# Performance work log

Hardware: AMD Instinct MI355X
Metric: run time of the kernel (lower is better)

The kernel has to match this reference:

```python
import jax, jax.numpy as jnp
import numpy as np

N_NODES = 50000
N_EDGES = 800000
IN_F = 256
OUT_F = 64


def setup_inputs() -> dict:
    key = jax.random.key(0)
    k1, k2, k3, k4, k5 = jax.random.split(key, 5)
    x = jax.random.normal(k1, (N_NODES, IN_F), dtype=jnp.float32)
    # xavier-uniform-like init for weight
    limit = float(np.sqrt(6.0 / (IN_F + OUT_F)))
    weight = jax.random.uniform(k2, (IN_F, OUT_F), dtype=jnp.float32, minval=-limit, maxval=limit)
    bias = jnp.zeros((1, OUT_F), dtype=jnp.float32)
    edge_weight = jax.random.uniform(k3, (N_EDGES,), dtype=jnp.float32)
    edge_src = jax.random.randint(k4, (N_EDGES,), 0, N_NODES, dtype=jnp.int32)
    edge_dst = jax.random.randint(k5, (N_EDGES,), 0, N_NODES, dtype=jnp.int32)
    return {"x": x, "weight": weight, "bias": bias,
            "edge_weight": edge_weight, "edge_src": edge_src, "edge_dst": edge_dst}


def reference(x, weight, bias, edge_weight, edge_src, edge_dst):
    # in_features (256) > out_features (64): transform first, then propagate.
    h = x @ weight                                  # [N, out]
    # spmm with COO adjacency: out[dst] += w_e * h[src]
    msgs = h[edge_src] * edge_weight[:, None]       # [E, out]
    out = jax.ops.segment_sum(msgs, edge_dst, num_segments=x.shape[0])  # [N, out]
    return out + bias
```

## Files before the change

### kernel.cpp

```cpp
#include <hip/hip_runtime.h>
#include <hip/hip_bf16.h>

#define N_NODES 50000
#define N_EDGES 800000
#define IN_F 256
#define OUT_F 64

#define CAP 64
#define NBKT 128
#define DST_PER_BKT 391
#define BKT_CAP 6912

typedef __attribute__((ext_vector_type(8))) short short8;
typedef __attribute__((ext_vector_type(4))) float f32x4;

static __device__ __forceinline__ ushort f2bf(float v) {
    __hip_bfloat16 b = __float2bfloat16(v);
    return *(ushort*)&b;
}

__global__ __launch_bounds__(256) void gc_prep(const float* __restrict__ W,
                                               ushort* __restrict__ Wb,
                                               int* __restrict__ cursor) {
    const int g = blockIdx.x * 256 + threadIdx.x;
    if (g < NBKT) cursor[g] = 0;
    {
        const int s = g >> 9;
        const int kk = (g >> 6) & 7;
        const int lane = g & 63;
        const int n = s * 16 + (lane & 15);
        const int kb = kk * 32 + (lane >> 4) * 8;
#pragma unroll
        for (int j = 0; j < 8; ++j)
            Wb[(size_t)g * 8 + j] = f2bf(W[(kb + j) * OUT_F + n]);
    }
}

__global__ __launch_bounds__(256) void gc_mid(const float* __restrict__ x,
                                              const ushort* __restrict__ Wb,
                                              ushort* __restrict__ h,
                                              const int* __restrict__ esrc,
                                              const int* __restrict__ edst,
                                              const float* __restrict__ ew,
                                              int* __restrict__ cursor,
                                              uint2* __restrict__ arena) {
    __shared__ ushort xs[32 * 264];
    __shared__ int hist[NBKT];
    __shared__ int base[NBKT];
    const int t = threadIdx.x;

    if (blockIdx.x < 391) {
        if (t < NBKT) hist[t] = 0;
        __syncthreads();

        const int e0 = blockIdx.x * 2048 + t * 8;
        const bool valid = e0 < N_EDGES;
        int b[8], loff[8];
        uint2 ent[8];
        if (valid) {
            const int4 sa = *(const int4*)(esrc + e0);
            const int4 sb = *(const int4*)(esrc + e0 + 4);
            const int4 da = *(const int4*)(edst + e0);
            const int4 db = *(const int4*)(edst + e0 + 4);
            const float4 wa = *(const float4*)(ew + e0);
            const float4 wb = *(const float4*)(ew + e0 + 4);
            const int ds[8] = {da.x, da.y, da.z, da.w, db.x, db.y, db.z, db.w};
            const int ss[8] = {sa.x, sa.y, sa.z, sa.w, sb.x, sb.y, sb.z, sb.w};
            const float wf[8] = {wa.x, wa.y, wa.z, wa.w, wb.x, wb.y, wb.z, wb.w};
#pragma unroll
            for (int j = 0; j < 8; ++j) {
                b[j] = ds[j] / DST_PER_BKT;
                ent[j].x = (unsigned)ds[j];
                ent[j].y = ((unsigned)f2bf(wf[j]) << 16) | (unsigned)(ss[j] & 0xFFFF);
                loff[j] = atomicAdd(&hist[b[j]], 1);
            }
        }
        __syncthreads();
        if (t < NBKT) {
            const int hc = hist[t];
            base[t] = hc ? atomicAdd(&cursor[t], hc) : 0;
        }
        __syncthreads();
        if (valid) {
#pragma unroll
            for (int j = 0; j < 8; ++j)
                arena[(size_t)b[j] * BKT_CAP + base[b[j]] + loff[j]] = ent[j];
        }
        return;
    }

    const int nbase = (blockIdx.x - 391) * 32;
    {
#pragma unroll
        for (int i = 0; i < 8; ++i) {
            const int idx = t + i * 256;
            const int node = idx >> 6;
            const int c4 = idx & 63;
            int gnode = nbase + node;
            if (gnode >= N_NODES) gnode = N_NODES - 1;
            const float4 v = ((const float4*)x)[(size_t)gnode * 64 + c4];
            ushort4 bv;
            bv.x = f2bf(v.x); bv.y = f2bf(v.y); bv.z = f2bf(v.z); bv.w = f2bf(v.w);
            *(ushort4*)&xs[node * 264 + c4 * 4] = bv;
        }
    }

    const int s = t >> 6;
    const int lane = t & 63;
    const int m = lane & 15;
    const int quad = lane >> 4;

    short8 bfrag[8];
#pragma unroll
    for (int kk = 0; kk < 8; ++kk)
        bfrag[kk] = *(const short8*)(Wb + ((size_t)(s * 8 + kk) * 64 + lane) * 8);

    __syncthreads();

    f32x4 acc0 = {0.f, 0.f, 0.f, 0.f};
    f32x4 acc1 = {0.f, 0.f, 0.f, 0.f};
#pragma unroll
    for (int kk = 0; kk < 8; ++kk) {
        const short8 a0 = *(const short8*)&xs[m * 264 + kk * 32 + quad * 8];
        const short8 a1 = *(const short8*)&xs[(16 + m) * 264 + kk * 32 + quad * 8];
        acc0 = __builtin_amdgcn_mfma_f32_16x16x32_bf16(a0, bfrag[kk], acc0, 0, 0, 0);
        acc1 = __builtin_amdgcn_mfma_f32_16x16x32_bf16(a1, bfrag[kk], acc1, 0, 0, 0);
    }

#pragma unroll
    for (int r = 0; r < 4; ++r) {
        const int row0 = nbase + quad * 4 + r;
        const int row1 = row0 + 16;
        if (row0 < N_NODES) h[(size_t)row0 * OUT_F + s * 16 + m] = f2bf(acc0[r]);
        if (row1 < N_NODES) h[(size_t)row1 * OUT_F + s * 16 + m] = f2bf(acc1[r]);
    }
}

__global__ __launch_bounds__(512) void gc_place2(const uint2* __restrict__ arena,
                                                 const int* __restrict__ cursor,
                                                 int* __restrict__ cnt,
                                                 unsigned int* __restrict__ slots) {
    __shared__ int lcnt[DST_PER_BKT];
    const int b = blockIdx.x;
    const int t = threadIdx.x;
    const int dbase = b * DST_PER_BKT;

    for (int i = t; i < DST_PER_BKT; i += 512) lcnt[i] = 0;
    __syncthreads();

    const int n = min(cursor[b], BKT_CAP);
    const uint2* __restrict__ p = arena + (size_t)b * BKT_CAP;
    for (int i = t; i < n; i += 512) {
        const uint2 ent = p[i];
        const int pos = atomicAdd(&lcnt[ent.x - dbase], 1);
        if (pos < CAP) slots[(size_t)ent.x * CAP + pos] = ent.y;
    }
    __syncthreads();

    for (int i = t; i < DST_PER_BKT; i += 512) {
        const int d = dbase + i;
        if (d < N_NODES) cnt[d] = lcnt[i];
    }
}

__global__ __launch_bounds__(256) void gc_gather(const ushort* __restrict__ h,
                                                 const unsigned int* __restrict__ slots,
                                                 const int* __restrict__ cnt,
                                                 const float* __restrict__ bias,
                                                 float* __restrict__ out) {
    const int wid = (blockIdx.x * 256 + threadIdx.x) >> 6;
    const int l = threadIdx.x & 63;
    const int d0 = wid * 4;

    const int4 c4 = *(const int4*)(cnt + d0);
    const int dg0 = min(c4.x, CAP), dg1 = min(c4.y, CAP);
    const int dg2 = min(c4.z, CAP), dg3 = min(c4.w, CAP);
    const int mdeg = max(max(dg0, dg1), max(dg2, dg3));

    const unsigned sw0 = (l < dg0) ? slots[(size_t)(d0 + 0) * CAP + l] : 0u;
    const unsigned sw1 = (l < dg1) ? slots[(size_t)(d0 + 1) * CAP + l] : 0u;
    const unsigned sw2 = (l < dg2) ? slots[(size_t)(d0 + 2) * CAP + l] : 0u;
    const unsigned sw3 = (l < dg3) ? slots[(size_t)(d0 + 3) * CAP + l] : 0u;

    const int es = l >> 3;
    const int fb = l & 7;

    float a0[8] = {0,0,0,0,0,0,0,0}, a1[8] = {0,0,0,0,0,0,0,0};
    float a2[8] = {0,0,0,0,0,0,0,0}, a3[8] = {0,0,0,0,0,0,0,0};

    const uint4* __restrict__ hb = (const uint4*)h;

    for (int i0 = 0; i0 < mdeg; i0 += 8) {
        const int ei = i0 + es;
        const unsigned q0 = (unsigned)__shfl((int)sw0, ei);
        const unsigned q1 = (unsigned)__shfl((int)sw1, ei);
        const unsigned q2 = (unsigned)__shfl((int)sw2, ei);
        const unsigned q3 = (unsigned)__shfl((int)sw3, ei);
        const uint4 v0 = hb[(size_t)(q0 & 0xFFFFu) * 8 + fb];
        const uint4 v1 = hb[(size_t)(q1 & 0xFFFFu) * 8 + fb];
        const uint4 v2 = hb[(size_t)(q2 & 0xFFFFu) * 8 + fb];
        const uint4 v3 = hb[(size_t)(q3 & 0xFFFFu) * 8 + fb];

#define FMA8(acc, q, v)                                                       \
    {                                                                         \
        const float w_ = __uint_as_float((q) & 0xFFFF0000u);                  \
        acc[0] = fmaf(w_, __uint_as_float((v).x << 16), acc[0]);              \
        acc[1] = fmaf(w_, __uint_as_float((v).x & 0xFFFF0000u), acc[1]);      \
        acc[2] = fmaf(w_, __uint_as_float((v).y << 16), acc[2]);              \
        acc[3] = fmaf(w_, __uint_as_float((v).y & 0xFFFF0000u), acc[3]);      \
        acc[4] = fmaf(w_, __uint_as_float((v).z << 16), acc[4]);              \
        acc[5] = fmaf(w_, __uint_as_float((v).z & 0xFFFF0000u), acc[5]);      \
        acc[6] = fmaf(w_, __uint_as_float((v).w << 16), acc[6]);              \
        acc[7] = fmaf(w_, __uint_as_float((v).w & 0xFFFF0000u), acc[7]);      \
    }
        FMA8(a0, q0, v0);
        FMA8(a1, q1, v1);
        FMA8(a2, q2, v2);
        FMA8(a3, q3, v3);
#undef FMA8
    }

#pragma unroll
    for (int k = 0; k < 8; ++k) {
        a0[k] += __shfl_xor(a0[k], 8); a0[k] += __shfl_xor(a0[k], 16); a0[k] += __shfl_xor(a0[k], 32);
        a1[k] += __shfl_xor(a1[k], 8); a1[k] += __shfl_xor(a1[k], 16); a1[k] += __shfl_xor(a1[k], 32);
        a2[k] += __shfl_xor(a2[k], 8); a2[k] += __shfl_xor(a2[k], 16); a2[k] += __shfl_xor(a2[k], 32);
        a3[k] += __shfl_xor(a3[k], 8); a3[k] += __shfl_xor(a3[k], 16); a3[k] += __shfl_xor(a3[k], 32);
    }

    if (l < 8) {
        const float4 ba = ((const float4*)bias)[l * 2];
        const float4 bb = ((const float4*)bias)[l * 2 + 1];
#define STORE4(acc, d)                                                        \
    {                                                                         \
        float4 oa, ob;                                                        \
        oa.x = acc[0] + ba.x; oa.y = acc[1] + ba.y;                           \
        oa.z = acc[2] + ba.z; oa.w = acc[3] + ba.w;                           \
        ob.x = acc[4] + bb.x; ob.y = acc[5] + bb.y;                           \
        ob.z = acc[6] + bb.z; ob.w = acc[7] + bb.w;                           \
        float4* op = (float4*)(out + (size_t)(d) * OUT_F + l * 8);            \
        op[0] = oa; op[1] = ob;                                               \
    }
        STORE4(a0, d0 + 0);
        STORE4(a1, d0 + 1);
        STORE4(a2, d0 + 2);
        STORE4(a3, d0 + 3);
#undef STORE4
    }
}

extern "C" void kernel_launch(void* const* d_in, const int* in_sizes, int n_in,
                              void* d_out, int out_size, void* d_ws, size_t ws_size,
                              hipStream_t stream) {
    const float* x    = (const float*)d_in[0];
    const float* W    = (const float*)d_in[1];
    const float* bias = (const float*)d_in[2];
    const float* ew   = (const float*)d_in[3];
    const int* src    = (const int*)d_in[4];
    const int* dst    = (const int*)d_in[5];
    float* out = (float*)d_out;

    char* ws = (char*)d_ws;
    ushort* h           = (ushort*)ws;
    int* cnt            = (int*)(ws + 6400000);
    unsigned int* slots = (unsigned int*)(ws + 6600000);
    ushort* Wb          = (ushort*)(ws + 19400000);
    int* cursor         = (int*)(ws + 19432768);
    uint2* arena        = (uint2*)(ws + 19433280);

    gc_prep<<<8, 256, 0, stream>>>(W, Wb, cursor);
    gc_mid<<<1954, 256, 0, stream>>>(x, Wb, h, src, dst, ew, cursor, arena);
    gc_place2<<<NBKT, 512, 0, stream>>>(arena, cursor, cnt, slots);
    gc_gather<<<3125, 256, 0, stream>>>(h, slots, cnt, bias, out);
}
```

Baseline: 145.3 us.

## Fuse slot placement and gather into per-bucket LDS atomic accumulation kernel

Replaces the two-pass place/gather scheme (per-destination slot table plus a separate gather kernel) with one kernel per destination bucket. It reads bucketed edges, gathers bf16 h rows and accumulates weighted messages with shared-memory float atomics into a 196x64 tile, then adds bias and writes the tile out. The bucket count is doubled so the tile fits in LDS. This removes the slots/cnt round trip through global memory and one launch. In exchange it has only 256 blocks of 1024 threads with heavy LDS usage, which limits occupancy, and it relies on LDS atomic contention staying low. It also drops the per-node degree cap, and edges that overflow a bucket's capacity are now silently discarded.

Measured after the change: 385.3 us. 165% more time.

```diff
diff --git a/kernel.cpp b/kernel.cpp
--- a/kernel.cpp
+++ b/kernel.cpp
@@ -6,10 +6,9 @@
 #define IN_F 256
 #define OUT_F 64
 
-#define CAP 64
-#define NBKT 128
-#define DST_PER_BKT 391
-#define BKT_CAP 6912
+#define NBKT 256
+#define DST_PER_BKT 196
+#define BKT_CAP 3584
 
 typedef __attribute__((ext_vector_type(8))) short short8;
 typedef __attribute__((ext_vector_type(4))) float f32x4;
@@ -83,8 +82,11 @@
         __syncthreads();
         if (valid) {
 #pragma unroll
-            for (int j = 0; j < 8; ++j)
-                arena[(size_t)b[j] * BKT_CAP + base[b[j]] + loff[j]] = ent[j];
+            for (int j = 0; j < 8; ++j) {
+                const int pos = base[b[j]] + loff[j];
+                if (pos < BKT_CAP)
+                    arena[(size_t)b[j] * BKT_CAP + pos] = ent[j];
+            }
         }
         return;
     }
@@ -136,116 +138,53 @@
     }
 }
 
-__global__ __launch_bounds__(512) void gc_place2(const uint2* __restrict__ arena,
+__global__ __launch_bounds__(1024) void gc_accum(const ushort* __restrict__ h,
+                                                 const uint2* __restrict__ arena,
                                                  const int* __restrict__ cursor,
-                                                 int* __restrict__ cnt,
-                                                 unsigned int* __restrict__ slots) {
-    __shared__ int lcnt[DST_PER_BKT];
+                                                 const float* __restrict__ bias,
+                                                 float* __restrict__ out) {
+    __shared__ float acc[DST_PER_BKT * OUT_F];
     const int b = blockIdx.x;
     const int t = threadIdx.x;
+    const int f = t & 63;
+    const int wav = t >> 6;
     const int dbase = b * DST_PER_BKT;
 
-    for (int i = t; i < DST_PER_BKT; i += 512) lcnt[i] = 0;
+    for (int i = t; i < DST_PER_BKT * OUT_F; i += 1024) acc[i] = 0.f;
     __syncthreads();
 
     const int n = min(cursor[b], BKT_CAP);
     const uint2* __restrict__ p = arena + (size_t)b * BKT_CAP;
-    for (int i = t; i < n; i += 512) {
-        const uint2 ent = p[i];
-        const int pos = atomicAdd(&lcnt[ent.x - dbase], 1);
-        if (pos < CAP) slots[(size_t)ent.x * CAP + pos] = ent.y;
+
+    for (int i0 = wav * 64; i0 < n; i0 += 16 * 64) {
+        const int idx = i0 + f;
+        uint2 ent = {(unsigned)dbase, 0u};
+        if (idx < n) ent = p[idx];
+
+#pragma unroll
+        for (int g = 0; g < 8; ++g) {
+            unsigned ex[8], ey[8];
+            ushort hv[8];
+#pragma unroll
+            for (int j = 0; j < 8; ++j) {
+                ex[j] = (unsigned)__builtin_amdgcn_readlane((int)ent.x, g * 8 + j);
+                ey[j] = (unsigned)__builtin_amdgcn_readlane((int)ent.y, g * 8 + j);
+                hv[j] = h[(size_t)(ey[j] & 0xFFFFu) * OUT_F + f];
+            }
+#pragma unroll
+            for (int j = 0; j < 8; ++j) {
+                const float w = __uint_as_float(ey[j] & 0xFFFF0000u);
+                const float v = __uint_as_float((unsigned)hv[j] << 16);
+                atomicAdd(&acc[(ex[j] - (unsigned)dbase) * OUT_F + f], w * v);
+            }
+        }
     }
     __syncthreads();
 
-    for (int i = t; i < DST_PER_BKT; i += 512) {
-        const int d = dbase + i;
-        if (d < N_NODES) cnt[d] = lcnt[i];
-    }
-}
-
-__global__ __launch_bounds__(256) void gc_gather(const ushort* __restrict__ h,
-                                                 const unsigned int* __restrict__ slots,
-                                                 const int* __restrict__ cnt,
-                                                 const float* __restrict__ bias,
-                                                 float* __restrict__ out) {
-    const int wid = (blockIdx.x * 256 + threadIdx.x) >> 6;
-    const int l = threadIdx.x & 63;
-    const int d0 = wid * 4;
-
-    const int4 c4 = *(const int4*)(cnt + d0);
-    const int dg0 = min(c4.x, CAP), dg1 = min(c4.y, CAP);
-    const int dg2 = min(c4.z, CAP), dg3 = min(c4.w, CAP);
-    const int mdeg = max(max(dg0, dg1), max(dg2, dg3));
-
-    const unsigned sw0 = (l < dg0) ? slots[(size_t)(d0 + 0) * CAP + l] : 0u;
-    const unsigned sw1 = (l < dg1) ? slots[(size_t)(d0 + 1) * CAP + l] : 0u;
-    const unsigned sw2 = (l < dg2) ? slots[(size_t)(d0 + 2) * CAP + l] : 0u;
-    const unsigned sw3 = (l < dg3) ? slots[(size_t)(d0 + 3) * CAP + l] : 0u;
-
-    const int es = l >> 3;
-    const int fb = l & 7;
-
-    float a0[8] = {0,0,0,0,0,0,0,0}, a1[8] = {0,0,0,0,0,0,0,0};
-    float a2[8] = {0,0,0,0,0,0,0,0}, a3[8] = {0,0,0,0,0,0,0,0};
-
-    const uint4* __restrict__ hb = (const uint4*)h;
-
-    for (int i0 = 0; i0 < mdeg; i0 += 8) {
-        const int ei = i0 + es;
-        const unsigned q0 = (unsigned)__shfl((int)sw0, ei);
-        const unsigned q1 = (unsigned)__shfl((int)sw1, ei);
-        const unsigned q2 = (unsigned)__shfl((int)sw2, ei);
-        const unsigned q3 = (unsigned)__shfl((int)sw3, ei);
-        const uint4 v0 = hb[(size_t)(q0 & 0xFFFFu) * 8 + fb];
-        const uint4 v1 = hb[(size_t)(q1 & 0xFFFFu) * 8 + fb];
-        const uint4 v2 = hb[(size_t)(q2 & 0xFFFFu) * 8 + fb];
-        const uint4 v3 = hb[(size_t)(q3 & 0xFFFFu) * 8 + fb];
-
-#define FMA8(acc, q, v)                                                       \
-    {                                                                         \
-        const float w_ = __uint_as_float((q) & 0xFFFF0000u);                  \
-        acc[0] = fmaf(w_, __uint_as_float((v).x << 16), acc[0]);              \
-        acc[1] = fmaf(w_, __uint_as_float((v).x & 0xFFFF0000u), acc[1]);      \
-        acc[2] = fmaf(w_, __uint_as_float((v).y << 16), acc[2]);              \
-        acc[3] = fmaf(w_, __uint_as_float((v).y & 0xFFFF0000u), acc[3]);      \
-        acc[4] = fmaf(w_, __uint_as_float((v).z << 16), acc[4]);              \
-        acc[5] = fmaf(w_, __uint_as_float((v).z & 0xFFFF0000u), acc[5]);      \
-        acc[6] = fmaf(w_, __uint_as_float((v).w << 16), acc[6]);              \
-        acc[7] = fmaf(w_, __uint_as_float((v).w & 0xFFFF0000u), acc[7]);      \
-    }
-        FMA8(a0, q0, v0);
-        FMA8(a1, q1, v1);
-        FMA8(a2, q2, v2);
-        FMA8(a3, q3, v3);
-#undef FMA8
-    }
-
-#pragma unroll
-    for (int k = 0; k < 8; ++k) {
-        a0[k] += __shfl_xor(a0[k], 8); a0[k] += __shfl_xor(a0[k], 16); a0[k] += __shfl_xor(a0[k], 32);
-        a1[k] += __shfl_xor(a1[k], 8); a1[k] += __shfl_xor(a1[k], 16); a1[k] += __shfl_xor(a1[k], 32);
-        a2[k] += __shfl_xor(a2[k], 8); a2[k] += __shfl_xor(a2[k], 16); a2[k] += __shfl_xor(a2[k], 32);
-        a3[k] += __shfl_xor(a3[k], 8); a3[k] += __shfl_xor(a3[k], 16); a3[k] += __shfl_xor(a3[k], 32);
-    }
-
-    if (l < 8) {
-        const float4 ba = ((const float4*)bias)[l * 2];
-        const float4 bb = ((const float4*)bias)[l * 2 + 1];
-#define STORE4(acc, d)                                                        \
-    {                                                                         \
-        float4 oa, ob;                                                        \
-        oa.x = acc[0] + ba.x; oa.y = acc[1] + ba.y;                           \
-        oa.z = acc[2] + ba.z; oa.w = acc[3] + ba.w;                           \
-        ob.x = acc[4] + bb.x; ob.y = acc[5] + bb.y;                           \
-        ob.z = acc[6] + bb.z; ob.w = acc[7] + bb.w;                           \
-        float4* op = (float4*)(out + (size_t)(d) * OUT_F + l * 8);            \
-        op[0] = oa; op[1] = ob;                                               \
-    }
-        STORE4(a0, d0 + 0);
-        STORE4(a1, d0 + 1);
-        STORE4(a2, d0 + 2);
-        STORE4(a3, d0 + 3);
-#undef STORE4
+    const float bf = bias[f];
+    for (int i = t; i < DST_PER_BKT * OUT_F; i += 1024) {
+        const int d = dbase + (i >> 6);
+        if (d < N_NODES) out[(size_t)d * OUT_F + (i & 63)] = acc[i] + bf;
     }
 }
 
@@ -261,15 +200,12 @@
     float* out = (float*)d_out;
 
     char* ws = (char*)d_ws;
-    ushort* h           = (ushort*)ws;
-    int* cnt            = (int*)(ws + 6400000);
-    unsigned int* slots = (unsigned int*)(ws + 6600000);
-    ushort* Wb          = (ushort*)(ws + 19400000);
-    int* cursor         = (int*)(ws + 19432768);
-    uint2* arena        = (uint2*)(ws + 19433280);
+    ushort* h    = (ushort*)ws;
+    ushort* Wb   = (ushort*)(ws + 6400000);
+    int* cursor  = (int*)(ws + 6432768);
+    uint2* arena = (uint2*)(ws + 6433792);
 
     gc_prep<<<8, 256, 0, stream>>>(W, Wb, cursor);
     gc_mid<<<1954, 256, 0, stream>>>(x, Wb, h, src, dst, ew, cursor, arena);
-    gc_place2<<<NBKT, 512, 0, stream>>>(arena, cursor, cnt, slots);
-    gc_gather<<<3125, 256, 0, stream>>>(h, slots, cnt, bias, out);
-}
+    gc_accum<<<NBKT, 1024, 0, stream>>>(h, arena, cursor, bias, out);
+}
```
